# Performance work log

Hardware: AMD Instinct MI355X
Metric: run time of the kernel (lower is better)

The kernel has to match this reference:

```python
import jax, jax.numpy as jnp
import numpy as np
from jax.ops import segment_sum

N = 100000      # nodes
E = 1600000     # edges (avg degree 16)
F_IN = 100      # data.num_features
D1 = 64         # dim1
D2 = 64         # dim2
CONV = 4        # conv_count
FC = 2          # fc_count
G = 500         # graphs in batch


def setup_inputs() -> dict:
    key = jax.random.key(0)
    ks = jax.random.split(key, 16)
    inp = {}
    inp['x'] = jax.random.normal(ks[0], (N, F_IN), dtype=jnp.float32)
    inp['edge_index'] = jax.random.randint(ks[1], (2, E), 0, N, dtype=jnp.int64)
    inp['edge_weight'] = jax.random.uniform(ks[2], (E,), dtype=jnp.float32)
    inp['batch'] = jnp.sort(jax.random.randint(ks[3], (N,), 0, G, dtype=jnp.int64))
    s = 0.05
    inp['lin0_w'] = jax.random.normal(ks[4], (F_IN, D1), dtype=jnp.float32) * s
    inp['lin0_b'] = jnp.zeros((D1,), dtype=jnp.float32)
    inp['conv_w'] = jax.random.normal(ks[5], (CONV, D1, D1), dtype=jnp.float32) * s
    inp['conv_b'] = jnp.zeros((CONV, D1), dtype=jnp.float32)
    inp['lin1_w'] = jax.random.normal(ks[6], (D1, D2), dtype=jnp.float32) * s
    inp['lin1_b'] = jnp.zeros((D2,), dtype=jnp.float32)
    inp['fc_w'] = jax.random.normal(ks[7], (FC, D2, D2), dtype=jnp.float32) * s
    inp['fc_b'] = jnp.zeros((FC, D2), dtype=jnp.float32)
    inp['lin2_w'] = jax.random.normal(ks[8], (D2, 1), dtype=jnp.float32) * s
    inp['lin2_b'] = jnp.zeros((1,), dtype=jnp.float32)
    return inp


def reference(x, edge_index, edge_weight, batch,
              lin0_w, lin0_b, conv_w, conv_b,
              lin1_w, lin1_b, fc_w, fc_b, lin2_w, lin2_b):
    row, col = edge_index[0], edge_index[1]  # source -> target

    # GCN symmetric normalization (add_self_loops=False, so 'improved' is a no-op)
    deg = segment_sum(edge_weight, col, num_segments=N)          # [N]
    dis = jnp.where(deg > 0, jax.lax.rsqrt(deg), 0.0)            # deg^{-1/2}, inf->0
    norm = dis[row] * edge_weight * dis[col]                     # [E]

    out = jax.nn.relu(x @ lin0_w + lin0_b)                       # [N, D1]
    for i in range(CONV):
        h = out @ conv_w[i]                                      # [N, D1]
        msg = h[row] * norm[:, None]                             # gather + scale, [E, D1]
        agg = segment_sum(msg, col, num_segments=N)              # scatter-add, [N, D1]
        out = jax.nn.relu(agg + conv_b[i])

    # global_mean_pool over graph ids
    sums = segment_sum(out, batch, num_segments=G)               # [G, D1]
    cnt = segment_sum(jnp.ones((N,), dtype=out.dtype), batch, num_segments=G)
    pooled = sums / jnp.clip(cnt, 1.0)[:, None]

    out = jax.nn.relu(pooled @ lin1_w + lin1_b)                  # [G, D2]
    for i in range(FC):
        out = jax.nn.relu(out @ fc_w[i] + fc_b[i])
    out = out @ lin2_w + lin2_b                                  # [G, 1]
    return out.reshape(-1)                                       # [G]
```

## Files before the change

### kernel.cpp

```cpp
#include <hip/hip_runtime.h>

#define NN 100000
#define NE 1600000
#define FIN 100
#define D 64
#define NCONV 4
#define NG 500

#define NB 196
#define BSH 9
#define EPB 2048
#define NBLKA ((NE + EPB - 1) / EPB)
#define NSCAN (NB * NBLKA)
#define SB 512
#define NBLKS ((NSCAN + SB - 1) / SB)

#define LSTR 136

typedef unsigned int uint;
typedef unsigned short ushort;
typedef __attribute__((ext_vector_type(8))) short bf16x8;
typedef __attribute__((ext_vector_type(4))) float f32x4;

__device__ inline ushort f2bf(float x) {
    uint u = __float_as_uint(x);
    u += 0x7fffu + ((u >> 16) & 1u);
    return (ushort)(u >> 16);
}
__device__ inline float bflo(uint u) { return __uint_as_float(u << 16); }
__device__ inline float bfhi(uint u) { return __uint_as_float(u & 0xffff0000u); }
__device__ inline float bf2f(ushort s) { return __uint_as_float((uint)s << 16); }

__global__ __launch_bounds__(256) void k_hist(const int* __restrict__ col,
                                              int* __restrict__ ghist) {
    __shared__ int lh[NB];
    int t = threadIdx.x;
    if (t < NB) lh[t] = 0;
    __syncthreads();
    int base = blockIdx.x * EPB;
    #pragma unroll
    for (int i = 0; i < 8; ++i) {
        int e = base + i * 256 + t;
        if (e < NE) atomicAdd(&lh[col[e] >> BSH], 1);
    }
    __syncthreads();
    if (t < NB) ghist[t * NBLKA + blockIdx.x] = lh[t];
}

__global__ __launch_bounds__(SB) void s_scan1(const int* __restrict__ in,
                                              int* __restrict__ out,
                                              int* __restrict__ bsums, int n) {
    __shared__ int sh[SB];
    int t = threadIdx.x, i = blockIdx.x * SB + t;
    int v = (i < n) ? in[i] : 0;
    sh[t] = v;
    __syncthreads();
    for (int off = 1; off < SB; off <<= 1) {
        int u = (t >= off) ? sh[t - off] : 0;
        __syncthreads();
        sh[t] += u;
        __syncthreads();
    }
    if (i < n) out[i] = sh[t] - v;
    if (t == SB - 1) bsums[blockIdx.x] = sh[t];
}

__global__ __launch_bounds__(SB) void s_scan2(int* __restrict__ bsums, int nb) {
    __shared__ int sh[SB];
    int t = threadIdx.x;
    int v = (t < nb) ? bsums[t] : 0;
    sh[t] = v;
    __syncthreads();
    for (int off = 1; off < SB; off <<= 1) {
        int u = (t >= off) ? sh[t - off] : 0;
        __syncthreads();
        sh[t] += u;
        __syncthreads();
    }
    if (t < nb) bsums[t] = sh[t] - v;
}

__global__ __launch_bounds__(SB) void s_scan3(int* __restrict__ out,
                                              const int* __restrict__ bsums, int n) {
    int i = blockIdx.x * SB + threadIdx.x;
    if (i < n) out[i] += bsums[blockIdx.x];
}

__global__ __launch_bounds__(256) void k_scatter(const int* __restrict__ row,
                                                 const int* __restrict__ col,
                                                 const float* __restrict__ ew,
                                                 const int* __restrict__ gscan,
                                                 int2* __restrict__ sorted) {
    __shared__ int lcur[NB];
    int t = threadIdx.x;
    if (t < NB) lcur[t] = gscan[t * NBLKA + blockIdx.x];
    __syncthreads();
    int base = blockIdx.x * EPB;
    #pragma unroll
    for (int i = 0; i < 8; ++i) {
        int e = base + i * 256 + t;
        if (e < NE) {
            int c = col[e];
            int pos = atomicAdd(&lcur[c >> BSH], 1);
            sorted[pos] = make_int2(row[e] | ((c & 511) << 17), __float_as_int(ew[e]));
        }
    }
}

__global__ __launch_bounds__(SB) void k_bcsr(const int2* __restrict__ sorted,
                                             const int* __restrict__ gscan,
                                             int* __restrict__ rowstart,
                                             int2* __restrict__ csr) {
    __shared__ int lcnt[SB];
    __shared__ int lscan[SB];
    int t = threadIdx.x, b = blockIdx.x;
    int base = gscan[b * NBLKA];
    int end  = (b == NB - 1) ? NE : gscan[(b + 1) * NBLKA];
    lcnt[t] = 0;
    __syncthreads();
    for (int e = base + t; e < end; e += SB)
        atomicAdd(&lcnt[sorted[e].x >> 17], 1);
    __syncthreads();
    int v = lcnt[t];
    lscan[t] = v;
    __syncthreads();
    for (int off = 1; off < SB; off <<= 1) {
        int u = (t >= off) ? lscan[t - off] : 0;
        __syncthreads();
        lscan[t] += u;
        __syncthreads();
    }
    int ex = lscan[t] - v;
    int idx = b * SB + t;
    if (idx <= NN) rowstart[idx] = base + ex;
    lcnt[t] = base + ex;
    __syncthreads();
    for (int e = base + t; e < end; e += SB) {
        int2 p = sorted[e];
        int slot = atomicAdd(&lcnt[p.x >> 17], 1);
        csr[slot] = make_int2(p.x & 0x1FFFF, p.y);
    }
}

__global__ __launch_bounds__(256) void k_rowdeg(const int2* __restrict__ csr,
                                                const int* __restrict__ rowstart,
                                                float* __restrict__ dis) {
    int t = threadIdx.x;
    int node = blockIdx.x * 16 + (t >> 4);
    int f = t & 15;
    int e0 = rowstart[node], e1 = rowstart[node + 1];
    float d = 0.f;
    for (int e = e0 + f; e < e1; e += 16) d += __int_as_float(csr[e].y);
    d += __shfl_xor(d, 1);
    d += __shfl_xor(d, 2);
    d += __shfl_xor(d, 4);
    d += __shfl_xor(d, 8);
    if (f == 0) dis[node] = (d > 0.f) ? (1.0f / sqrtf(d)) : 0.f;
}

__global__ __launch_bounds__(256) void k_rownorm(int2* __restrict__ csr,
                                                 const int* __restrict__ rowstart,
                                                 const float* __restrict__ dis) {
    int t = threadIdx.x;
    int node = blockIdx.x * 16 + (t >> 4);
    int f = t & 15;
    int e0 = rowstart[node], e1 = rowstart[node + 1];
    float dc = dis[node];
    for (int e = e0 + f; e < e1; e += 16) {
        int2 p = csr[e];
        float w = dis[p.x] * __int_as_float(p.y) * dc;
        csr[e] = make_int2(p.x, __float_as_int(w));
    }
}

__global__ void k_wsplit(const float* __restrict__ conv_w, ushort* __restrict__ wf) {
    int tid = blockIdx.x * blockDim.x + threadIdx.x;
    int j = tid & 7;
    int lane = (tid >> 3) & 63;
    int kh = (tid >> 9) & 1;
    int ct = (tid >> 10) & 3;
    int l = tid >> 12;
    int k = kh * 32 + (lane >> 4) * 8 + j;
    int n = ct * 16 + (lane & 15);
    float w = conv_w[l * D * D + k * D + n];
    ushort hi = f2bf(w);
    ushort lo = f2bf(w - bf2f(hi));
    int base = (((l * 4 + ct) * 2 + kh) * 2) * 512 + lane * 8 + j;
    wf[base] = hi;
    wf[base + 512] = lo;
}

__global__ void k_wsplit0(const float* __restrict__ w, ushort* __restrict__ wf) {
    int tid = blockIdx.x * blockDim.x + threadIdx.x;
    int j = tid & 7;
    int lane = (tid >> 3) & 63;
    int ks = (tid >> 9) & 3;
    int ct = tid >> 11;
    int k = ks * 32 + (lane >> 4) * 8 + j;
    int n = ct * 16 + (lane & 15);
    float v = (k < FIN) ? w[k * D + n] : 0.f;
    ushort hi = f2bf(v);
    ushort lo = f2bf(v - bf2f(hi));
    int base = ((ct * 4 + ks) * 2) * 512 + lane * 8 + j;
    wf[base] = hi;
    wf[base + 512] = lo;
}

__global__ __launch_bounds__(256) void k_lin0_mfma(const float* __restrict__ x,
                                                   const ushort* __restrict__ wf,
                                                   const float* __restrict__ b,
                                                   ushort* __restrict__ out) {
    __shared__ ushort xhi[64 * LSTR];
    __shared__ ushort xlo[64 * LSTR];
    int t = threadIdx.x;
    int r0 = blockIdx.x * 64;
    for (int i = t; i < 1600; i += 256) {
        int r = i / 25, c4 = i - (i / 25) * 25;
        float4 v = {0.f, 0.f, 0.f, 0.f};
        if (r0 + r < NN)
            v = *reinterpret_cast<const float4*>(&x[(size_t)(r0 + r) * FIN + c4 * 4]);
        int base = r * LSTR + c4 * 4;
        ushort h;
        h = f2bf(v.x); xhi[base + 0] = h; xlo[base + 0] = f2bf(v.x - bf2f(h));
        h = f2bf(v.y); xhi[base + 1] = h; xlo[base + 1] = f2bf(v.y - bf2f(h));
        h = f2bf(v.z); xhi[base + 2] = h; xlo[base + 2] = f2bf(v.z - bf2f(h));
        h = f2bf(v.w); xhi[base + 3] = h; xlo[base + 3] = f2bf(v.w - bf2f(h));
    }
    for (int i = t; i < 64 * 28; i += 256) {
        int r = i / 28, c = FIN + (i - (i / 28) * 28);
        xhi[r * LSTR + c] = 0;
        xlo[r * LSTR + c] = 0;
    }
    __syncthreads();
    int wave = t >> 6, lane = t & 63;
    int lrow = wave * 16 + (lane & 15);
    bf16x8 ahi[4], alo[4];
    #pragma unroll
    for (int ks = 0; ks < 4; ++ks) {
        int off = lrow * LSTR + ks * 32 + (lane >> 4) * 8;
        ahi[ks] = *reinterpret_cast<const bf16x8*>(&xhi[off]);
        alo[ks] = *reinterpret_cast<const bf16x8*>(&xlo[off]);
    }
    float bv[4];
    #pragma unroll
    for (int ct = 0; ct < 4; ++ct) bv[ct] = b[ct * 16 + (lane & 15)];
    int r = r0 + wave * 16;
    f32x4 acc[4];
    #pragma unroll
    for (int ct = 0; ct < 4; ++ct) {
        acc[ct] = {bv[ct], bv[ct], bv[ct], bv[ct]};
        #pragma unroll
        for (int ks = 0; ks < 4; ++ks) {
            int base = ((ct * 4 + ks) * 2) * 512 + lane * 8;
            bf16x8 wh = *reinterpret_cast<const bf16x8*>(&wf[base]);
            bf16x8 wl = *reinterpret_cast<const bf16x8*>(&wf[base + 512]);
            acc[ct] = __builtin_amdgcn_mfma_f32_16x16x32_bf16(ahi[ks], wh, acc[ct], 0, 0, 0);
            acc[ct] = __builtin_amdgcn_mfma_f32_16x16x32_bf16(ahi[ks], wl, acc[ct], 0, 0, 0);
            acc[ct] = __builtin_amdgcn_mfma_f32_16x16x32_bf16(alo[ks], wh, acc[ct], 0, 0, 0);
        }
    }
    #pragma unroll
    for (int ct = 0; ct < 4; ++ct) {
        int ocol = ct * 16 + (lane & 15);
        #pragma unroll
        for (int i = 0; i < 4; ++i) {
            int orow = r + (lane >> 4) * 4 + i;
            if (orow < NN) out[orow * D + ocol] = f2bf(fmaxf(acc[ct][i], 0.f));
        }
    }
}

__global__ __launch_bounds__(256, 8) void k_agg(const ushort* __restrict__ src,
                                                const int* __restrict__ rowstart,
                                                const int2* __restrict__ csr,
                                                ushort* __restrict__ dst) {
    int t = threadIdx.x;
    int lane = t & 63;
    int g = lane >> 4;
    int f = lane & 15;
    int node = blockIdx.x * 16 + (t >> 6) * 4 + g;
    int e0 = rowstart[node], e1 = rowstart[node + 1];
    float4 acc = {0.f, 0.f, 0.f, 0.f};
    int2 p0, p1, p2, p3;
    {
        int a0 = e0 + 0 < e1 ? e0 + 0 : 0;
        int a1 = e0 + 1 < e1 ? e0 + 1 : 0;
        int a2 = e0 + 2 < e1 ? e0 + 2 : 0;
        int a3 = e0 + 3 < e1 ? e0 + 3 : 0;
        p0 = csr[a0]; p1 = csr[a1]; p2 = csr[a2]; p3 = csr[a3];
    }
    for (int base = e0; base < e1; base += 4) {
        int n0 = base + 4 < e1 ? base + 4 : 0;
        int n1 = base + 5 < e1 ? base + 5 : 0;
        int n2 = base + 6 < e1 ? base + 6 : 0;
        int n3 = base + 7 < e1 ? base + 7 : 0;
        int2 q0 = csr[n0], q1 = csr[n1], q2 = csr[n2], q3 = csr[n3];
        float w0 = (base + 0 < e1) ? __int_as_float(p0.y) : 0.f;
        float w1 = (base + 1 < e1) ? __int_as_float(p1.y) : 0.f;
        float w2 = (base + 2 < e1) ? __int_as_float(p2.y) : 0.f;
        float w3 = (base + 3 < e1) ? __int_as_float(p3.y) : 0.f;
        uint2 v0 = *reinterpret_cast<const uint2*>(&src[p0.x * D + f * 4]);
        uint2 v1 = *reinterpret_cast<const uint2*>(&src[p1.x * D + f * 4]);
        uint2 v2 = *reinterpret_cast<const uint2*>(&src[p2.x * D + f * 4]);
        uint2 v3 = *reinterpret_cast<const uint2*>(&src[p3.x * D + f * 4]);
        acc.x = fmaf(bflo(v0.x), w0, acc.x); acc.y = fmaf(bfhi(v0.x), w0, acc.y);
        acc.z = fmaf(bflo(v0.y), w0, acc.z); acc.w = fmaf(bfhi(v0.y), w0, acc.w);
        acc.x = fmaf(bflo(v1.x), w1, acc.x); acc.y = fmaf(bfhi(v1.x), w1, acc.y);
        acc.z = fmaf(bflo(v1.y), w1, acc.z); acc.w = fmaf(bfhi(v1.y), w1, acc.w);
        acc.x = fmaf(bflo(v2.x), w2, acc.x); acc.y = fmaf(bfhi(v2.x), w2, acc.y);
        acc.z = fmaf(bflo(v2.y), w2, acc.z); acc.w = fmaf(bfhi(v2.y), w2, acc.w);
        acc.x = fmaf(bflo(v3.x), w3, acc.x); acc.y = fmaf(bfhi(v3.x), w3, acc.y);
        acc.z = fmaf(bflo(v3.y), w3, acc.z); acc.w = fmaf(bfhi(v3.y), w3, acc.w);
        p0 = q0; p1 = q1; p2 = q2; p3 = q3;
    }
    uint2 o;
    o.x = (uint)f2bf(acc.x) | ((uint)f2bf(acc.y) << 16);
    o.y = (uint)f2bf(acc.z) | ((uint)f2bf(acc.w) << 16);
    *reinterpret_cast<uint2*>(&dst[node * D + f * 4]) = o;
}

__global__ __launch_bounds__(256) void k_mfma_dense(const ushort* __restrict__ a,
                                                    const ushort* __restrict__ wf,
                                                    const float* __restrict__ bias,
                                                    ushort* __restrict__ out) {
    int t = threadIdx.x;
    int wave = t >> 6, lane = t & 63;
    bf16x8 wh[4][2], wl[4][2];
    #pragma unroll
    for (int ct = 0; ct < 4; ++ct)
        #pragma unroll
        for (int kh = 0; kh < 2; ++kh) {
            int base = ((ct * 2 + kh) * 2) * 512 + lane * 8;
            wh[ct][kh] = *reinterpret_cast<const bf16x8*>(&wf[base]);
            wl[ct][kh] = *reinterpret_cast<const bf16x8*>(&wf[base + 512]);
        }
    float bias_v[4];
    #pragma unroll
    for (int ct = 0; ct < 4; ++ct) bias_v[ct] = bias[ct * 16 + (lane & 15)];

    int r = blockIdx.x * 64 + wave * 16;
    if (r >= NN) return;
    int arow = r + (lane & 15);
    bf16x8 a0 = *reinterpret_cast<const bf16x8*>(&a[arow * D + (lane >> 4) * 8]);
    bf16x8 a1 = *reinterpret_cast<const bf16x8*>(&a[arow * D + 32 + (lane >> 4) * 8]);

    f32x4 acc[4];
    #pragma unroll
    for (int ct = 0; ct < 4; ++ct) {
        acc[ct] = {bias_v[ct], bias_v[ct], bias_v[ct], bias_v[ct]};
        acc[ct] = __builtin_amdgcn_mfma_f32_16x16x32_bf16(a0, wh[ct][0], acc[ct], 0, 0, 0);
        acc[ct] = __builtin_amdgcn_mfma_f32_16x16x32_bf16(a1, wh[ct][1], acc[ct], 0, 0, 0);
        acc[ct] = __builtin_amdgcn_mfma_f32_16x16x32_bf16(a0, wl[ct][0], acc[ct], 0, 0, 0);
        acc[ct] = __builtin_amdgcn_mfma_f32_16x16x32_bf16(a1, wl[ct][1], acc[ct], 0, 0, 0);
    }
    #pragma unroll
    for (int ct = 0; ct < 4; ++ct) {
        int ocol = ct * 16 + (lane & 15);
        #pragma unroll
        for (int i = 0; i < 4; ++i) {
            int orow = r + (lane >> 4) * 4 + i;
            out[orow * D + ocol] = f2bf(fmaxf(acc[ct][i], 0.f));
        }
    }
}

__global__ __launch_bounds__(256) void k_pool(const ushort* __restrict__ src,
                                              const int* __restrict__ batch,
                                              float* __restrict__ pooled,
                                              float* __restrict__ cnt) {
    int wave = threadIdx.x >> 6, lane = threadIdx.x & 63;
    int n0 = blockIdx.x * 64 + wave * 16;
    float s = 0.f;
    int curg = -1, runlen = 0;
    for (int i = 0; i < 16; ++i) {
        int node = n0 + i;
        if (node >= NN) break;
        int gg = batch[node];
        if (gg != curg) {
            if (curg >= 0) {
                atomicAdd(&pooled[curg * D + lane], s);
                if (lane == 0) atomicAdd(&cnt[curg], (float)runlen);
            }
            curg = gg; s = 0.f; runlen = 0;
        }
        s += bf2f(src[node * D + lane]);
        ++runlen;
    }
    if (curg >= 0) {
        atomicAdd(&pooled[curg * D + lane], s);
        if (lane == 0) atomicAdd(&cnt[curg], (float)runlen);
    }
}

__global__ __launch_bounds__(64) void k_head(const float* __restrict__ pooled,
                                             const float* __restrict__ cnt,
                                             const float* __restrict__ lin1_w,
                                             const float* __restrict__ lin1_b,
                                             const float* __restrict__ fc_w,
                                             const float* __restrict__ fc_b,
                                             const float* __restrict__ lin2_w,
                                             const float* __restrict__ lin2_b,
                                             float* __restrict__ out) {
    __shared__ float buf0[D], buf1[D];
    int g = blockIdx.x, d = threadIdx.x;
    float c = fmaxf(cnt[g], 1.0f);
    buf0[d] = pooled[g * D + d] / c;
    __syncthreads();
    float acc = lin1_b[d];
    #pragma unroll
    for (int k = 0; k < D; ++k) acc += buf0[k] * lin1_w[k * D + d];
    buf1[d] = fmaxf(acc, 0.f);
    __syncthreads();
    acc = fc_b[d];
    #pragma unroll
    for (int k = 0; k < D; ++k) acc += buf1[k] * fc_w[k * D + d];
    buf0[d] = fmaxf(acc, 0.f);
    __syncthreads();
    acc = fc_b[D + d];
    #pragma unroll
    for (int k = 0; k < D; ++k) acc += buf0[k] * fc_w[D * D + k * D + d];
    buf1[d] = fmaxf(acc, 0.f);
    __syncthreads();
    float v = buf1[d] * lin2_w[d];
    #pragma unroll
    for (int off = 32; off; off >>= 1) v += __shfl_down(v, off);
    if (d == 0) out[g] = v + lin2_b[0];
}

extern "C" void kernel_launch(void* const* d_in, const int* in_sizes, int n_in,
                              void* d_out, int out_size, void* d_ws, size_t ws_size,
                              hipStream_t stream) {
    const float* x      = (const float*)d_in[0];
    const int*   ei     = (const int*)  d_in[1];
    const float* ew     = (const float*)d_in[2];
    const int*   batch  = (const int*)  d_in[3];
    const float* lin0_w = (const float*)d_in[4];
    const float* lin0_b = (const float*)d_in[5];
    const float* conv_w = (const float*)d_in[6];
    const float* conv_b = (const float*)d_in[7];
    const float* lin1_w = (const float*)d_in[8];
    const float* lin1_b = (const float*)d_in[9];
    const float* fc_w   = (const float*)d_in[10];
    const float* fc_b   = (const float*)d_in[11];
    const float* lin2_w = (const float*)d_in[12];
    const float* lin2_b = (const float*)d_in[13];
    float* out = (float*)d_out;

    const int* rowv = ei;
    const int* colv = ei + NE;

    ushort* bufA    = (ushort*)d_ws;
    ushort* bufB    = bufA + (size_t)NN * D;
    ushort* bufG    = bufB + (size_t)NN * D;
    int2*   csr     = (int2*)(bufG + (size_t)NN * D);
    int*   rowstart = (int*)(csr + NE);
    float* dis      = (float*)(rowstart + NN + 1);
    float* pooled   = dis + NN;
    float* cnt      = pooled + NG * D;
    ushort* wfrags  = (ushort*)(cnt + NG);
    ushort* wfrags0 = wfrags + 4 * 8192;
    int2*  sorted   = (int2*)bufG;
    int*   ghist    = (int*)bufB;
    int*   gscan    = ghist + NSCAN;
    int*   bsums    = gscan + NSCAN;

    hipMemsetAsync(pooled, 0, (NG * D + NG) * sizeof(float), stream);

    k_hist<<<NBLKA, 256, 0, stream>>>(colv, ghist);
    s_scan1<<<NBLKS, SB, 0, stream>>>(ghist, gscan, bsums, NSCAN);
    s_scan2<<<1, SB, 0, stream>>>(bsums, NBLKS);
    s_scan3<<<NBLKS, SB, 0, stream>>>(gscan, bsums, NSCAN);
    k_scatter<<<NBLKA, 256, 0, stream>>>(rowv, colv, ew, gscan, sorted);
    k_bcsr<<<NB, SB, 0, stream>>>(sorted, gscan, rowstart, csr);

    k_rowdeg<<<NN / 16, 256, 0, stream>>>(csr, rowstart, dis);
    k_rownorm<<<NN / 16, 256, 0, stream>>>(csr, rowstart, dis);
    k_wsplit<<<64, 256, 0, stream>>>(conv_w, wfrags);
    k_wsplit0<<<32, 256, 0, stream>>>(lin0_w, wfrags0);

    k_lin0_mfma<<<(NN + 63) / 64, 256, 0, stream>>>(x, wfrags0, lin0_b, bufA);

    int dg = (NN + 63) / 64;
    k_agg<<<NN / 16, 256, 0, stream>>>(bufA, rowstart, csr, bufG);
    k_mfma_dense<<<dg, 256, 0, stream>>>(bufG, wfrags + 0 * 8192, conv_b + 0 * D, bufB);
    k_agg<<<NN / 16, 256, 0, stream>>>(bufB, rowstart, csr, bufG);
    k_mfma_dense<<<dg, 256, 0, stream>>>(bufG, wfrags + 1 * 8192, conv_b + 1 * D, bufA);
    k_agg<<<NN / 16, 256, 0, stream>>>(bufA, rowstart, csr, bufG);
    k_mfma_dense<<<dg, 256, 0, stream>>>(bufG, wfrags + 2 * 8192, conv_b + 2 * D, bufB);
    k_agg<<<NN / 16, 256, 0, stream>>>(bufB, rowstart, csr, bufG);
    k_mfma_dense<<<dg, 256, 0, stream>>>(bufG, wfrags + 3 * 8192, conv_b + 3 * D, bufA);

    k_pool<<<(NN + 63) / 64, 256, 0, stream>>>(bufA, batch, pooled, cnt);
    k_head<<<NG, 64, 0, stream>>>(pooled, cnt, lin1_w, lin1_b, fc_w, fc_b,
                                  lin2_w, lin2_b, out);
}
```

Baseline: 302.9 us.

## Fuse neighbor aggregation with dense conv matmul via shared-memory staging

Merges the per-layer gather/aggregate kernel and the MFMA dense transform into one kernel. Each block aggregates 16 nodes, stages the bf16 rows in LDS, then each wave computes one 16-column tile of the 64x64 weight product with bias and ReLU. This removes the intermediate global write and read of the aggregated features and halves the launches per conv layer. In exchange it adds a block barrier, and each block reloads its weight fragments from global memory.

```diff
diff --git a/kernel.cpp b/kernel.cpp
--- a/kernel.cpp
+++ b/kernel.cpp
@@ -16,6 +16,7 @@
 #define NBLKS ((NSCAN + SB - 1) / SB)
 
 #define LSTR 136
+#define ASTR 72
 
 typedef unsigned int uint;
 typedef unsigned short ushort;
@@ -270,15 +271,19 @@
     }
 }
 
-__global__ __launch_bounds__(256, 8) void k_agg(const ushort* __restrict__ src,
-                                                const int* __restrict__ rowstart,
-                                                const int2* __restrict__ csr,
-                                                ushort* __restrict__ dst) {
-    int t = threadIdx.x;
-    int lane = t & 63;
+__global__ __launch_bounds__(256, 8) void k_conv_fused(const ushort* __restrict__ src,
+                                                       const int* __restrict__ rowstart,
+                                                       const int2* __restrict__ csr,
+                                                       const ushort* __restrict__ wf,
+                                                       const float* __restrict__ bias,
+                                                       ushort* __restrict__ dst) {
+    __shared__ ushort arow[16 * ASTR];
+    int t = threadIdx.x;
+    int wave = t >> 6, lane = t & 63;
     int g = lane >> 4;
     int f = lane & 15;
-    int node = blockIdx.x * 16 + (t >> 6) * 4 + g;
+    int rloc = wave * 4 + g;
+    int node = blockIdx.x * 16 + rloc;
     int e0 = rowstart[node], e1 = rowstart[node + 1];
     float4 acc = {0.f, 0.f, 0.f, 0.f};
     int2 p0, p1, p2, p3;
@@ -316,51 +321,30 @@
     uint2 o;
     o.x = (uint)f2bf(acc.x) | ((uint)f2bf(acc.y) << 16);
     o.y = (uint)f2bf(acc.z) | ((uint)f2bf(acc.w) << 16);
-    *reinterpret_cast<uint2*>(&dst[node * D + f * 4]) = o;
-}
-
-__global__ __launch_bounds__(256) void k_mfma_dense(const ushort* __restrict__ a,
-                                                    const ushort* __restrict__ wf,
-                                                    const float* __restrict__ bias,
-                                                    ushort* __restrict__ out) {
-    int t = threadIdx.x;
-    int wave = t >> 6, lane = t & 63;
-    bf16x8 wh[4][2], wl[4][2];
-    #pragma unroll
-    for (int ct = 0; ct < 4; ++ct)
-        #pragma unroll
-        for (int kh = 0; kh < 2; ++kh) {
-            int base = ((ct * 2 + kh) * 2) * 512 + lane * 8;
-            wh[ct][kh] = *reinterpret_cast<const bf16x8*>(&wf[base]);
-            wl[ct][kh] = *reinterpret_cast<const bf16x8*>(&wf[base + 512]);
-        }
-    float bias_v[4];
-    #pragma unroll
-    for (int ct = 0; ct < 4; ++ct) bias_v[ct] = bias[ct * 16 + (lane & 15)];
-
-    int r = blockIdx.x * 64 + wave * 16;
-    if (r >= NN) return;
-    int arow = r + (lane & 15);
-    bf16x8 a0 = *reinterpret_cast<const bf16x8*>(&a[arow * D + (lane >> 4) * 8]);
-    bf16x8 a1 = *reinterpret_cast<const bf16x8*>(&a[arow * D + 32 + (lane >> 4) * 8]);
-
-    f32x4 acc[4];
-    #pragma unroll
-    for (int ct = 0; ct < 4; ++ct) {
-        acc[ct] = {bias_v[ct], bias_v[ct], bias_v[ct], bias_v[ct]};
-        acc[ct] = __builtin_amdgcn_mfma_f32_16x16x32_bf16(a0, wh[ct][0], acc[ct], 0, 0, 0);
-        acc[ct] = __builtin_amdgcn_mfma_f32_16x16x32_bf16(a1, wh[ct][1], acc[ct], 0, 0, 0);
-        acc[ct] = __builtin_amdgcn_mfma_f32_16x16x32_bf16(a0, wl[ct][0], acc[ct], 0, 0, 0);
-        acc[ct] = __builtin_amdgcn_mfma_f32_16x16x32_bf16(a1, wl[ct][1], acc[ct], 0, 0, 0);
-    }
-    #pragma unroll
-    for (int ct = 0; ct < 4; ++ct) {
-        int ocol = ct * 16 + (lane & 15);
-        #pragma unroll
-        for (int i = 0; i < 4; ++i) {
-            int orow = r + (lane >> 4) * 4 + i;
-            out[orow * D + ocol] = f2bf(fmaxf(acc[ct][i], 0.f));
-        }
+    *reinterpret_cast<uint2*>(&arow[rloc * ASTR + f * 4]) = o;
+    __syncthreads();
+    int ct = wave;
+    int base0 = ((ct * 2 + 0) * 2) * 512 + lane * 8;
+    int base1 = ((ct * 2 + 1) * 2) * 512 + lane * 8;
+    bf16x8 wh0 = *reinterpret_cast<const bf16x8*>(&wf[base0]);
+    bf16x8 wl0 = *reinterpret_cast<const bf16x8*>(&wf[base0 + 512]);
+    bf16x8 wh1 = *reinterpret_cast<const bf16x8*>(&wf[base1]);
+    bf16x8 wl1 = *reinterpret_cast<const bf16x8*>(&wf[base1 + 512]);
+    int arow_idx = lane & 15;
+    bf16x8 a0 = *reinterpret_cast<const bf16x8*>(&arow[arow_idx * ASTR + (lane >> 4) * 8]);
+    bf16x8 a1 = *reinterpret_cast<const bf16x8*>(&arow[arow_idx * ASTR + 32 + (lane >> 4) * 8]);
+    float bv = bias[ct * 16 + (lane & 15)];
+    f32x4 c = {bv, bv, bv, bv};
+    c = __builtin_amdgcn_mfma_f32_16x16x32_bf16(a0, wh0, c, 0, 0, 0);
+    c = __builtin_amdgcn_mfma_f32_16x16x32_bf16(a1, wh1, c, 0, 0, 0);
+    c = __builtin_amdgcn_mfma_f32_16x16x32_bf16(a0, wl0, c, 0, 0, 0);
+    c = __builtin_amdgcn_mfma_f32_16x16x32_bf16(a1, wl1, c, 0, 0, 0);
+    int ocol = ct * 16 + (lane & 15);
+    int r0 = blockIdx.x * 16;
+    #pragma unroll
+    for (int i = 0; i < 4; ++i) {
+        int orow = r0 + (lane >> 4) * 4 + i;
+        dst[orow * D + ocol] = f2bf(fmaxf(c[i], 0.f));
     }
 }
 
@@ -480,15 +464,15 @@
 
     k_lin0_mfma<<<(NN + 63) / 64, 256, 0, stream>>>(x, wfrags0, lin0_b, bufA);
 
-    int dg = (NN + 63) / 64;
-    k_agg<<<NN / 16, 256, 0, stream>>>(bufA, rowstart, csr, bufG);
-    k_mfma_dense<<<dg, 256, 0, stream>>>(bufG, wfrags + 0 * 8192, conv_b + 0 * D, bufB);
-    k_agg<<<NN / 16, 256, 0, stream>>>(bufB, rowstart, csr, bufG);
-    k_mfma_dense<<<dg, 256, 0, stream>>>(bufG, wfrags + 1 * 8192, conv_b + 1 * D, bufA);
-    k_agg<<<NN / 16, 256, 0, stream>>>(bufA, rowstart, csr, bufG);
-    k_mfma_dense<<<dg, 256, 0, stream>>>(bufG, wfrags + 2 * 8192, conv_b + 2 * D, bufB);
-    k_agg<<<NN / 16, 256, 0, stream>>>(bufB, rowstart, csr, bufG);
-    k_mfma_dense<<<dg, 256, 0, stream>>>(bufG, wfrags + 3 * 8192, conv_b + 3 * D, bufA);
+    int cg = NN / 16;
+    k_conv_fused<<<cg, 256, 0, stream>>>(bufA, rowstart, csr, wfrags + 0 * 8192,
+                                         conv_b + 0 * D, bufB);
+    k_conv_fused<<<cg, 256, 0, stream>>>(bufB, rowstart, csr, wfrags + 1 * 8192,
+                                         conv_b + 1 * D, bufA);
+    k_conv_fused<<<cg, 256, 0, stream>>>(bufA, rowstart, csr, wfrags + 2 * 8192,
+                                         conv_b + 2 * D, bufB);
+    k_conv_fused<<<cg, 256, 0, stream>>>(bufB, rowstart, csr, wfrags + 3 * 8192,
+                                         conv_b + 3 * D, bufA);
 
     k_pool<<<(NN + 63) / 64, 256, 0, stream>>>(bufA, batch, pooled, cnt);
     k_head<<<NG, 64, 0, stream>>>(pooled, cnt, lin1_w, lin1_b, fc_w, fc_b,
```

After: 280.1 us. -7.5%, faster.
